# Kernel tuning notes

Hardware: AMD Instinct MI355X
Metric: run time of the kernel (lower is better)

The kernel has to match this reference:

```python
import jax, jax.numpy as jnp
import numpy as np

B, C, H, W = 8, 64, 256, 256
WIN = 8
DEPTH = 1
SHIFT = WIN // 2
NH, NW = H // WIN, W // WIN
P = WIN * WIN  # tokens per window


def conv1x1(x, w):
    return jax.lax.conv_general_dilated(x, w, (1, 1), 'VALID',
                                        dimension_numbers=('NCHW', 'OIHW', 'NCHW'))


def dwconv3x3(x, w, groups):
    return jax.lax.conv_general_dilated(x, w, (1, 1), ((1, 1), (1, 1)),
                                        dimension_numbers=('NCHW', 'OIHW', 'NCHW'),
                                        feature_group_count=groups)


def l2norm(x, eps=1e-12):
    # matches torch.nn.functional.normalize(dim=-1)
    n = jnp.sqrt(jnp.sum(x * x, axis=-1, keepdims=True))
    return x / jnp.maximum(n, eps)


def setup_inputs() -> dict:
    key = jax.random.key(0)
    ks = jax.random.split(key, 5)
    x = jax.random.normal(ks[0], (B, C, H, W), dtype=jnp.float32)
    q = jax.random.normal(ks[1], (B, C, WIN, WIN), dtype=jnp.float32)
    kv_w = jax.random.normal(ks[2], (2 * C, C, 1, 1), dtype=jnp.float32) * 0.05
    dw_w = jax.random.normal(ks[3], (2 * C, 1, 3, 3), dtype=jnp.float32) * 0.05
    proj_w = jax.random.normal(ks[4], (C, C, 1, 1), dtype=jnp.float32) * 0.05
    rescale1 = jnp.ones((1, 1, 1), dtype=jnp.float32)
    rescale2 = jnp.ones((1, 1, 1), dtype=jnp.float32)
    return {'x': x, 'q': q, 'kv_w': kv_w, 'dw_w': dw_w, 'proj_w': proj_w,
            'rescale1': rescale1, 'rescale2': rescale2}


def reference(x, q, kv_w, dw_w, proj_w, rescale1, rescale2):
    if DEPTH % 2:
        x = jnp.roll(x, (-SHIFT, -SHIFT), axis=(2, 3))
    qf = q.reshape(B, C, P)
    xw = x.reshape(B, C, NH, WIN, NW, WIN).transpose(0, 2, 4, 1, 3, 5)
    xw = xw.reshape(B * NH * NW, C, WIN, WIN)
    kv = dwconv3x3(conv1x1(xw, kv_w), dw_w, 2 * C)
    kv = kv.reshape(B, NH * NW, 2 * C, P)
    k, v = kv[:, :, :C, :], kv[:, :, C:, :]
    qn = l2norm(qf)          # [B, C, P]
    kn = l2norm(k)           # [B, nW, C, P]
    # attn1 = k @ q^T : [B, nW, C, C]
    attn1 = jax.nn.softmax(jnp.einsum('bwcp,bdp->bwcd', kn, qn) * rescale1, axis=-1)
    out1 = jnp.einsum('bwcd,bwdp->bwcp', attn1, v)
    # attn2 = k @ v^T : [B, nW, C, C]
    attn2 = jax.nn.softmax(jnp.einsum('bwcp,bwdp->bwcd', kn, v) * rescale2, axis=-1)
    out2 = jnp.einsum('bwcd,bdp->bwcp', attn2, qn)
    f1 = jnp.fft.fft(out1.astype(jnp.complex64), axis=-1)
    f2 = jnp.fft.fft(out2.astype(jnp.complex64), axis=-1)
    o = jnp.fft.ifft(f1 + f2, axis=-1)
    out = (o.real + o.imag).astype(jnp.float32)  # [B, nW, C, P]
    # windows back to image: [B,C,H,W]
    out = out.reshape(B, NH, NW, C, WIN, WIN).transpose(0, 3, 1, 4, 2, 5)
    out = out.reshape(B, C, H, W)
    out = conv1x1(out, proj_w)
    if DEPTH % 2:
        out = jnp.roll(out, (SHIFT, SHIFT), axis=(2, 3))
    return out
```

## Files before the change

### kernel.cpp

```cpp
#include <hip/hip_runtime.h>
#include <math.h>


typedef __attribute__((ext_vector_type(8))) short short8;
typedef __attribute__((ext_vector_type(4))) float f32x4;

#define LSTR 72

__device__ __forceinline__ short f2bf(float f) {
    unsigned u = __float_as_uint(f);
    u = u + 0x7FFFu + ((u >> 16) & 1u);
    return (short)(u >> 16);
}
__device__ __forceinline__ void unpack8(short8 h, float* f) {
#pragma unroll
    for (int j = 0; j < 8; ++j) f[j] = __uint_as_float(((unsigned)(unsigned short)h[j]) << 16);
}

__global__ void prep(const float* __restrict__ q, const float* __restrict__ kvw,
                     const float* __restrict__ pjw, short* __restrict__ qn_dp,
                     short* __restrict__ qn_pd, short* __restrict__ kvw_bf,
                     short* __restrict__ pjw_bf) {
    int bid = blockIdx.x, t = threadIdx.x;
    if (bid < 512) {
        float v = q[bid * 64 + t];
        float s = v * v;
#pragma unroll
        for (int off = 32; off > 0; off >>= 1) s += __shfl_xor(s, off, 64);
        float inv = 1.0f / fmaxf(sqrtf(s), 1e-12f);
        short h = f2bf(v * inv);
        int b = bid >> 6, d = bid & 63;
        qn_dp[b * 4096 + d * 64 + t] = h;
        qn_pd[b * 4096 + t * 64 + d] = h;
    } else {
        int idx = (bid - 512) * 64 + t;
        if (idx < 8192) kvw_bf[idx] = f2bf(kvw[idx]);
        else if (idx < 12288) pjw_bf[idx - 8192] = f2bf(pjw[idx - 8192]);
    }
}

__global__ void __launch_bounds__(256, 2)
attn_main(const float* __restrict__ xg, const short* __restrict__ qn_dp,
          const short* __restrict__ qn_pd, const short* __restrict__ kvw_bf,
          const float* __restrict__ dww, const short* __restrict__ pjw_bf,
          const float* __restrict__ rs1p, const float* __restrict__ rs2p,
          float* __restrict__ outg) {
    __shared__ short Xs[64 * LSTR];
    __shared__ short Ts[64 * LSTR];
    __shared__ short KNs[64 * LSTR];
    __shared__ short Vs[64 * LSTR];
#define VTs Xs
#define A1s Ts

    const int tid = threadIdx.x;
    const int w = tid >> 6, lane = tid & 63, lg = lane >> 4, ln = lane & 15;
    const int b = blockIdx.x & 7;
    const int widx = blockIdx.x >> 3;
    const int wh = widx >> 5, ww = widx & 31;
    const float rs1 = rs1p[0], rs2 = rs2p[0];

    const short* qdp = qn_dp + b * 4096;
    const short* qpd = qn_pd + b * 4096;

#pragma unroll
    for (int rep = 0; rep < 2; ++rep) {
        int r = tid + rep * 256;
        int c = r >> 3, i = r & 7;
        int h = (wh * 8 + i + 4) & 255;
        const float* src = xg + (((b * 64 + c) * 256 + h) << 8);
        float4 av = *(const float4*)(src + ww * 8 + 4);
        float4 bv = *(const float4*)(src + ((ww * 8 + 8) & 255));
        float vals[8] = {av.x, av.y, av.z, av.w, bv.x, bv.y, bv.z, bv.w};
        int csw = ((((c >> 3) ^ i) & 7) << 3) | (c & 7);
#pragma unroll
        for (int j = 0; j < 8; ++j) Xs[(i * 8 + j) * LSTR + csw] = f2bf(vals[j]);
    }
    __syncthreads();

#pragma unroll 1
    for (int half = 0; half < 2; ++half) {
        {
            f32x4 acc[4] = {};
            const short* Wg = kvw_bf + half * 4096;
#pragma unroll
            for (int kc = 0; kc < 2; ++kc) {
                short8 af = *(const short8*)(Wg + (w * 16 + ln) * 64 + kc * 32 + lg * 8);
#pragma unroll
                for (int t = 0; t < 4; ++t) {
                    int row = t * 16 + ln;
                    short8 bf = *(const short8*)&Xs[row * LSTR + ((((kc * 4 + lg) ^ (row >> 3)) & 7) << 3)];
                    acc[t] = __builtin_amdgcn_mfma_f32_16x16x32_bf16(af, bf, acc[t], 0, 0, 0);
                }
            }
#pragma unroll
            for (int t = 0; t < 4; ++t)
#pragma unroll
                for (int r = 0; r < 4; ++r)
                    Ts[(w * 16 + lg * 4 + r) * LSTR + t * 16 + ln] = f2bf(acc[t][r]);
        }
        __syncthreads();

        {
            int o = tid >> 2, q = tid & 3;
            const float* wp = dww + (half * 64 + o) * 9;
            float wq[9];
#pragma unroll
            for (int k = 0; k < 9; ++k) wq[k] = wp[k];
            float rv[4][8];
#pragma unroll
            for (int dy = 0; dy < 4; ++dy) {
                int y = 2 * q - 1 + dy;
                if (y >= 0 && y < 8) {
                    short8 t8 = *(const short8*)&Ts[o * LSTR + y * 8];
                    unpack8(t8, rv[dy]);
                } else {
#pragma unroll
                    for (int j = 0; j < 8; ++j) rv[dy][j] = 0.f;
                }
            }
            float ov[16];
#pragma unroll
            for (int rr = 0; rr < 2; ++rr)
#pragma unroll
                for (int j = 0; j < 8; ++j) {
                    float a = 0.f;
#pragma unroll
                    for (int dy = 0; dy < 3; ++dy)
#pragma unroll
                        for (int dx = 0; dx < 3; ++dx) {
                            int xx = j + dx - 1;
                            if (xx >= 0 && xx < 8) a += wq[dy * 3 + dx] * rv[rr + dy][xx];
                        }
                    ov[rr * 8 + j] = a;
                }
            if (half == 0) {
                float ss = 0.f;
#pragma unroll
                for (int k = 0; k < 16; ++k) ss += ov[k] * ov[k];
                ss += __shfl_xor(ss, 1);
                ss += __shfl_xor(ss, 2);
                float inv = 1.0f / fmaxf(sqrtf(ss), 1e-12f);
                short8 h0, h1;
#pragma unroll
                for (int k = 0; k < 8; ++k) { h0[k] = f2bf(ov[k] * inv); h1[k] = f2bf(ov[k + 8] * inv); }
                *(short8*)&KNs[o * LSTR + q * 16] = h0;
                *(short8*)&KNs[o * LSTR + q * 16 + 8] = h1;
            } else {
                short8 h0, h1;
#pragma unroll
                for (int k = 0; k < 8; ++k) { h0[k] = f2bf(ov[k]); h1[k] = f2bf(ov[k + 8]); }
                *(short8*)&Vs[o * LSTR + q * 16] = h0;
                *(short8*)&Vs[o * LSTR + q * 16 + 8] = h1;
#pragma unroll
                for (int k = 0; k < 16; ++k) {
                    int p = q * 16 + k;
                    int csw = ((((o >> 3) ^ (p >> 3)) & 7) << 3) | (o & 7);
                    VTs[p * LSTR + csw] = (k < 8) ? h0[k] : h1[k - 8];
                }
            }
        }
        __syncthreads();
    }

    const int arow = (w * 16 + ln) * LSTR;
    const int crow = w * 16 + lg * 4;

    {
        f32x4 s1[4] = {};
#pragma unroll
        for (int kc = 0; kc < 2; ++kc) {
            short8 af = *(const short8*)&KNs[arow + kc * 32 + lg * 8];
#pragma unroll
            for (int t = 0; t < 4; ++t) {
                short8 fb = *(const short8*)(qdp + (t * 16 + ln) * 64 + kc * 32 + lg * 8);
                s1[t] = __builtin_amdgcn_mfma_f32_16x16x32_bf16(af, fb, s1[t], 0, 0, 0);
            }
        }
#pragma unroll
        for (int r = 0; r < 4; ++r) {
            float v0 = s1[0][r] * rs1, v1 = s1[1][r] * rs1, v2 = s1[2][r] * rs1, v3 = s1[3][r] * rs1;
            float m = fmaxf(fmaxf(v0, v1), fmaxf(v2, v3));
#pragma unroll
            for (int off = 1; off < 16; off <<= 1) m = fmaxf(m, __shfl_xor(m, off));
            float e0 = __expf(v0 - m), e1 = __expf(v1 - m), e2 = __expf(v2 - m), e3 = __expf(v3 - m);
            float s = e0 + e1 + e2 + e3;
#pragma unroll
            for (int off = 1; off < 16; off <<= 1) s += __shfl_xor(s, off);
            float inv = 1.0f / s;
            A1s[(crow + r) * LSTR + 0 * 16 + ln] = f2bf(e0 * inv);
            A1s[(crow + r) * LSTR + 1 * 16 + ln] = f2bf(e1 * inv);
            A1s[(crow + r) * LSTR + 2 * 16 + ln] = f2bf(e2 * inv);
            A1s[(crow + r) * LSTR + 3 * 16 + ln] = f2bf(e3 * inv);
        }
    }
    __syncthreads();

    f32x4 o1[4] = {};
    f32x4 s2[4] = {};
    {
#pragma unroll
        for (int kc = 0; kc < 2; ++kc) {
            short8 af = *(const short8*)&A1s[arow + kc * 32 + lg * 8];
#pragma unroll
            for (int t = 0; t < 4; ++t) {
                int row = t * 16 + ln;
                short8 bf = *(const short8*)&VTs[row * LSTR + ((((kc * 4 + lg) ^ (row >> 3)) & 7) << 3)];
                o1[t] = __builtin_amdgcn_mfma_f32_16x16x32_bf16(af, bf, o1[t], 0, 0, 0);
            }
        }
#pragma unroll
        for (int kc = 0; kc < 2; ++kc) {
            short8 af = *(const short8*)&KNs[arow + kc * 32 + lg * 8];
#pragma unroll
            for (int t = 0; t < 4; ++t) {
                short8 bf = *(const short8*)&Vs[(t * 16 + ln) * LSTR + kc * 32 + lg * 8];
                s2[t] = __builtin_amdgcn_mfma_f32_16x16x32_bf16(af, bf, s2[t], 0, 0, 0);
            }
        }
    }
    __syncthreads();

#pragma unroll
    for (int r = 0; r < 4; ++r) {
        float v0 = s2[0][r] * rs2, v1 = s2[1][r] * rs2, v2 = s2[2][r] * rs2, v3 = s2[3][r] * rs2;
        float m = fmaxf(fmaxf(v0, v1), fmaxf(v2, v3));
#pragma unroll
        for (int off = 1; off < 16; off <<= 1) m = fmaxf(m, __shfl_xor(m, off));
        float e0 = __expf(v0 - m), e1 = __expf(v1 - m), e2 = __expf(v2 - m), e3 = __expf(v3 - m);
        float s = e0 + e1 + e2 + e3;
#pragma unroll
        for (int off = 1; off < 16; off <<= 1) s += __shfl_xor(s, off);
        float inv = 1.0f / s;
        A1s[(crow + r) * LSTR + 0 * 16 + ln] = f2bf(e0 * inv);
        A1s[(crow + r) * LSTR + 1 * 16 + ln] = f2bf(e1 * inv);
        A1s[(crow + r) * LSTR + 2 * 16 + ln] = f2bf(e2 * inv);
        A1s[(crow + r) * LSTR + 3 * 16 + ln] = f2bf(e3 * inv);
    }
    __syncthreads();

    {
#pragma unroll
        for (int kc = 0; kc < 2; ++kc) {
            short8 af = *(const short8*)&A1s[arow + kc * 32 + lg * 8];
#pragma unroll
            for (int t = 0; t < 4; ++t) {
                short8 fb = *(const short8*)(qpd + (t * 16 + ln) * 64 + kc * 32 + lg * 8);
                o1[t] = __builtin_amdgcn_mfma_f32_16x16x32_bf16(af, fb, o1[t], 0, 0, 0);
            }
        }
#pragma unroll
        for (int t = 0; t < 4; ++t)
#pragma unroll
            for (int r = 0; r < 4; ++r) {
                int c = crow + r, p = t * 16 + ln;
                int csw = ((((c >> 3) ^ (p >> 3)) & 7) << 3) | (c & 7);
                Xs[p * LSTR + csw] = f2bf(o1[t][r]);
            }
    }
    __syncthreads();

    {
        f32x4 pr[4] = {};
#pragma unroll
        for (int kc = 0; kc < 2; ++kc) {
            short8 af = *(const short8*)(pjw_bf + (w * 16 + ln) * 64 + kc * 32 + lg * 8);
#pragma unroll
            for (int t = 0; t < 4; ++t) {
                int row = t * 16 + ln;
                short8 bf = *(const short8*)&Xs[row * LSTR + ((((kc * 4 + lg) ^ (row >> 3)) & 7) << 3)];
                pr[t] = __builtin_amdgcn_mfma_f32_16x16x32_bf16(af, bf, pr[t], 0, 0, 0);
            }
        }
#pragma unroll
        for (int t = 0; t < 4; ++t)
#pragma unroll
            for (int r = 0; r < 4; ++r) {
                int co = crow + r, p = t * 16 + ln;
                int h = (wh * 8 + (p >> 3) + 4) & 255;
                int wc = (ww * 8 + (p & 7) + 4) & 255;
                outg[((b * 64 + co) << 16) + (h << 8) + wc] = pr[t][r];
            }
    }
#undef VTs
#undef A1s
}

extern "C" void kernel_launch(void* const* d_in, const int* in_sizes, int n_in,
                              void* d_out, int out_size, void* d_ws, size_t ws_size,
                              hipStream_t stream) {
    const float* x = (const float*)d_in[0];
    const float* q = (const float*)d_in[1];
    const float* kvw = (const float*)d_in[2];
    const float* dww = (const float*)d_in[3];
    const float* pjw = (const float*)d_in[4];
    const float* rs1 = (const float*)d_in[5];
    const float* rs2 = (const float*)d_in[6];
    float* out = (float*)d_out;

    short* ws = (short*)d_ws;
    short* qn_dp = ws;
    short* qn_pd = ws + 32768;
    short* kvw_bf = ws + 65536;
    short* pjw_bf = ws + 73728;

    prep<<<dim3(704), dim3(64), 0, stream>>>(q, kvw, pjw, qn_dp, qn_pd, kvw_bf, pjw_bf);
    attn_main<<<dim3(8192), dim3(256), 0, stream>>>(x, qn_dp, qn_pd, kvw_bf, dww, pjw_bf,
                                                    rs1, rs2, out);
}
```

Measured before the change: 364.0 us.

## Reorder attention stages to drop two barriers and raise occupancy hint

Both softmaxes are now computed back to back, each wave working only on its own rows. The second attention matrix is written into the K buffer rows that wave owns, so the two barriers between the first softmax, the attn1·V / k·v products and the second softmax go away. The LDS buffers are reassigned so the buffers still being read are not overwritten before the next barrier. Launch bounds go from 2 to 4 blocks per CU, which caps registers harder and may cause spills in exchange for more resident waves to hide latency.

```diff
diff --git a/kernel.cpp b/kernel.cpp
--- a/kernel.cpp
+++ b/kernel.cpp
@@ -39,7 +39,7 @@
     }
 }
 
-__global__ void __launch_bounds__(256, 2)
+__global__ void __launch_bounds__(256, 4)
 attn_main(const float* __restrict__ xg, const short* __restrict__ qn_dp,
           const short* __restrict__ qn_pd, const short* __restrict__ kvw_bf,
           const float* __restrict__ dww, const short* __restrict__ pjw_bf,
@@ -49,8 +49,6 @@
     __shared__ short Ts[64 * LSTR];
     __shared__ short KNs[64 * LSTR];
     __shared__ short Vs[64 * LSTR];
-#define VTs Xs
-#define A1s Ts
 
     const int tid = threadIdx.x;
     const int w = tid >> 6, lane = tid & 63, lg = lane >> 4, ln = lane & 15;
@@ -155,7 +153,7 @@
                 for (int k = 0; k < 16; ++k) {
                     int p = q * 16 + k;
                     int csw = ((((o >> 3) ^ (p >> 3)) & 7) << 3) | (o & 7);
-                    VTs[p * LSTR + csw] = (k < 8) ? h0[k] : h1[k - 8];
+                    Xs[p * LSTR + csw] = (k < 8) ? h0[k] : h1[k - 8];
                 }
             }
         }
@@ -187,27 +185,14 @@
 #pragma unroll
             for (int off = 1; off < 16; off <<= 1) s += __shfl_xor(s, off);
             float inv = 1.0f / s;
-            A1s[(crow + r) * LSTR + 0 * 16 + ln] = f2bf(e0 * inv);
-            A1s[(crow + r) * LSTR + 1 * 16 + ln] = f2bf(e1 * inv);
-            A1s[(crow + r) * LSTR + 2 * 16 + ln] = f2bf(e2 * inv);
-            A1s[(crow + r) * LSTR + 3 * 16 + ln] = f2bf(e3 * inv);
-        }
-    }
-    __syncthreads();
-
-    f32x4 o1[4] = {};
-    f32x4 s2[4] = {};
+            Ts[(crow + r) * LSTR + 0 * 16 + ln] = f2bf(e0 * inv);
+            Ts[(crow + r) * LSTR + 1 * 16 + ln] = f2bf(e1 * inv);
+            Ts[(crow + r) * LSTR + 2 * 16 + ln] = f2bf(e2 * inv);
+            Ts[(crow + r) * LSTR + 3 * 16 + ln] = f2bf(e3 * inv);
+        }
+    }
     {
-#pragma unroll
-        for (int kc = 0; kc < 2; ++kc) {
-            short8 af = *(const short8*)&A1s[arow + kc * 32 + lg * 8];
-#pragma unroll
-            for (int t = 0; t < 4; ++t) {
-                int row = t * 16 + ln;
-                short8 bf = *(const short8*)&VTs[row * LSTR + ((((kc * 4 + lg) ^ (row >> 3)) & 7) << 3)];
-                o1[t] = __builtin_amdgcn_mfma_f32_16x16x32_bf16(af, bf, o1[t], 0, 0, 0);
-            }
-        }
+        f32x4 s2[4] = {};
 #pragma unroll
         for (int kc = 0; kc < 2; ++kc) {
             short8 af = *(const short8*)&KNs[arow + kc * 32 + lg * 8];
@@ -217,31 +202,40 @@
                 s2[t] = __builtin_amdgcn_mfma_f32_16x16x32_bf16(af, bf, s2[t], 0, 0, 0);
             }
         }
+#pragma unroll
+        for (int r = 0; r < 4; ++r) {
+            float v0 = s2[0][r] * rs2, v1 = s2[1][r] * rs2, v2 = s2[2][r] * rs2, v3 = s2[3][r] * rs2;
+            float m = fmaxf(fmaxf(v0, v1), fmaxf(v2, v3));
+#pragma unroll
+            for (int off = 1; off < 16; off <<= 1) m = fmaxf(m, __shfl_xor(m, off));
+            float e0 = __expf(v0 - m), e1 = __expf(v1 - m), e2 = __expf(v2 - m), e3 = __expf(v3 - m);
+            float s = e0 + e1 + e2 + e3;
+#pragma unroll
+            for (int off = 1; off < 16; off <<= 1) s += __shfl_xor(s, off);
+            float inv = 1.0f / s;
+            KNs[(crow + r) * LSTR + 0 * 16 + ln] = f2bf(e0 * inv);
+            KNs[(crow + r) * LSTR + 1 * 16 + ln] = f2bf(e1 * inv);
+            KNs[(crow + r) * LSTR + 2 * 16 + ln] = f2bf(e2 * inv);
+            KNs[(crow + r) * LSTR + 3 * 16 + ln] = f2bf(e3 * inv);
+        }
     }
     __syncthreads();
 
-#pragma unroll
-    for (int r = 0; r < 4; ++r) {
-        float v0 = s2[0][r] * rs2, v1 = s2[1][r] * rs2, v2 = s2[2][r] * rs2, v3 = s2[3][r] * rs2;
-        float m = fmaxf(fmaxf(v0, v1), fmaxf(v2, v3));
-#pragma unroll
-        for (int off = 1; off < 16; off <<= 1) m = fmaxf(m, __shfl_xor(m, off));
-        float e0 = __expf(v0 - m), e1 = __expf(v1 - m), e2 = __expf(v2 - m), e3 = __expf(v3 - m);
-        float s = e0 + e1 + e2 + e3;
-#pragma unroll
-        for (int off = 1; off < 16; off <<= 1) s += __shfl_xor(s, off);
-        float inv = 1.0f / s;
-        A1s[(crow + r) * LSTR + 0 * 16 + ln] = f2bf(e0 * inv);
-        A1s[(crow + r) * LSTR + 1 * 16 + ln] = f2bf(e1 * inv);
-        A1s[(crow + r) * LSTR + 2 * 16 + ln] = f2bf(e2 * inv);
-        A1s[(crow + r) * LSTR + 3 * 16 + ln] = f2bf(e3 * inv);
-    }
-    __syncthreads();
-
     {
-#pragma unroll
-        for (int kc = 0; kc < 2; ++kc) {
-            short8 af = *(const short8*)&A1s[arow + kc * 32 + lg * 8];
+        f32x4 o1[4] = {};
+#pragma unroll
+        for (int kc = 0; kc < 2; ++kc) {
+            short8 af = *(const short8*)&Ts[arow + kc * 32 + lg * 8];
+#pragma unroll
+            for (int t = 0; t < 4; ++t) {
+                int row = t * 16 + ln;
+                short8 bf = *(const short8*)&Xs[row * LSTR + ((((kc * 4 + lg) ^ (row >> 3)) & 7) << 3)];
+                o1[t] = __builtin_amdgcn_mfma_f32_16x16x32_bf16(af, bf, o1[t], 0, 0, 0);
+            }
+        }
+#pragma unroll
+        for (int kc = 0; kc < 2; ++kc) {
+            short8 af = *(const short8*)&KNs[arow + kc * 32 + lg * 8];
 #pragma unroll
             for (int t = 0; t < 4; ++t) {
                 short8 fb = *(const short8*)(qpd + (t * 16 + ln) * 64 + kc * 32 + lg * 8);
@@ -254,7 +248,7 @@
             for (int r = 0; r < 4; ++r) {
                 int c = crow + r, p = t * 16 + ln;
                 int csw = ((((c >> 3) ^ (p >> 3)) & 7) << 3) | (c & 7);
-                Xs[p * LSTR + csw] = f2bf(o1[t][r]);
+                Vs[p * LSTR + csw] = f2bf(o1[t][r]);
             }
     }
     __syncthreads();
@@ -267,7 +261,7 @@
 #pragma unroll
             for (int t = 0; t < 4; ++t) {
                 int row = t * 16 + ln;
-                short8 bf = *(const short8*)&Xs[row * LSTR + ((((kc * 4 + lg) ^ (row >> 3)) & 7) << 3)];
+                short8 bf = *(const short8*)&Vs[row * LSTR + ((((kc * 4 + lg) ^ (row >> 3)) & 7) << 3)];
                 pr[t] = __builtin_amdgcn_mfma_f32_16x16x32_bf16(af, bf, pr[t], 0, 0, 0);
             }
         }
@@ -281,8 +275,6 @@
                 outg[((b * 64 + co) << 16) + (h << 8) + wc] = pr[t][r];
             }
     }
-#undef VTs
-#undef A1s
 }
 
 extern "C" void kernel_launch(void* const* d_in, const int* in_sizes, int n_in,
```

After: 366.0 us. Within noise of the previous version (+0.6%).
